# Performance work log

Measured on AMD Instinct MI355X. Metric: run time of the kernel, lower is better.

## Reference

```python
import jax, jax.numpy as jnp
import numpy as np

N = 50000
E = 800000
DIMS = [(8, 16), (16, 16), (16, 16)]  # (in, out) per layer


def setup_inputs() -> dict:
    key = jax.random.key(0)
    ks = jax.random.split(key, 32)
    inp = {}
    inp['x'] = jax.random.normal(ks[0], (N, 8), dtype=jnp.float32)
    inp['pos'] = jax.random.normal(ks[1], (N, 3), dtype=jnp.float32)
    k = 2
    for i, (ci, co) in enumerate(DIMS):
        d = ci * co
        inp[f'lin_w{i}'] = jax.random.normal(ks[k], (3, d), dtype=jnp.float32); k += 1
        inp[f'lin_b{i}'] = jax.random.normal(ks[k], (d,), dtype=jnp.float32); k += 1
        inp[f'gamma{i}'] = jax.random.normal(ks[k], (d,), dtype=jnp.float32); k += 1
        inp[f'beta{i}'] = jax.random.normal(ks[k], (d,), dtype=jnp.float32); k += 1
        inp[f'root{i}'] = jax.random.normal(ks[k], (ci, co), dtype=jnp.float32); k += 1
        inp[f'bias{i}'] = jax.random.normal(ks[k], (co,), dtype=jnp.float32); k += 1
    inp['batch'] = jnp.zeros((N,), dtype=jnp.int32)
    inp['idx'] = jnp.sort(jax.random.randint(ks[k], (25000,), 0, N, dtype=jnp.int32)); k += 1
    inp['edge_index'] = jax.random.randint(ks[k], (2, E), 0, N, dtype=jnp.int32)
    return inp


def _nnconv(x, pseudo, src, dst, lin_w, lin_b, gamma, beta, root, bias, ci, co):
    # edge MLP (Linear -> batchnorm(eval, affine) -> ReLU), plain_last=False
    w = jax.nn.relu((pseudo @ lin_w + lin_b) * gamma + beta)  # [E, ci*co]
    w = w.reshape(-1, ci, co)                                  # [E, ci, co]
    msg = jnp.einsum('ei,eio->eo', x[src], w)                  # per-edge vec-mat
    s = jax.ops.segment_sum(msg, dst, num_segments=N)          # scatter-sum
    cnt = jax.ops.segment_sum(jnp.ones((msg.shape[0],), x.dtype), dst, num_segments=N)
    aggr = s / jnp.maximum(cnt, 1.0)[:, None]                  # scatter-mean
    return aggr + x @ root + bias


def reference(x, pos, lin_w0, lin_b0, gamma0, beta0, root0, bias0,
              lin_w1, lin_b1, gamma1, beta1, root1, bias1,
              lin_w2, lin_b2, gamma2, beta2, root2, bias2,
              batch, idx, edge_index):
    src, dst = edge_index[0], edge_index[1]
    pseudo = pos[dst] - pos[src]  # patch_size is None
    params = [
        (lin_w0, lin_b0, gamma0, beta0, root0, bias0),
        (lin_w1, lin_b1, gamma1, beta1, root1, bias1),
        (lin_w2, lin_b2, gamma2, beta2, root2, bias2),
    ]
    h = x
    for (ci, co), p in zip(DIMS, params):
        h = jax.nn.relu(_nnconv(h, pseudo, src, dst, *p, ci, co))  # drop_act=False
    return h[idx], pos[idx], batch[idx]
```

## Files before the change

### kernel.cpp

```cpp
#include <hip/hip_runtime.h>

#define N_NODES 50000
#define N_EDGES 800000
#define M_IDX   25000
#define DMAX    64

typedef float v2f __attribute__((ext_vector_type(2)));

__global__ __launch_bounds__(256) void prep_kernel(
    const int*   __restrict__ ei,
    const float* __restrict__ pos,
    int*         __restrict__ cnt,
    float4*      __restrict__ pdata,
    const float* __restrict__ lw0, const float* __restrict__ lb0,
    const float* __restrict__ g0,  const float* __restrict__ b0,
    const float* __restrict__ lw1, const float* __restrict__ lb1,
    const float* __restrict__ g1,  const float* __restrict__ b1,
    const float* __restrict__ lw2, const float* __restrict__ lb2,
    const float* __restrict__ g2,  const float* __restrict__ b2,
    float4*      __restrict__ wtab,
    int E)
{
    if (blockIdx.x < 3) {
        const int l = blockIdx.x, j = threadIdx.x;
        const float *lw, *lb, *gm, *bt; int d;
        if (l == 0)      { lw = lw0; lb = lb0; gm = g0; bt = b0; d = 128; }
        else if (l == 1) { lw = lw1; lb = lb1; gm = g1; bt = b1; d = 256; }
        else             { lw = lw2; lb = lb2; gm = g2; bt = b2; d = 256; }
        if (j < d) {
            const float g = gm[j];
            float4 w4;
            w4.x = lw[j] * g;
            w4.y = lw[d + j] * g;
            w4.z = lw[2 * d + j] * g;
            w4.w = fmaf(lb[j], g, bt[j]);
            wtab[l * 256 + j] = w4;
        }
    }

    const int e0 = blockIdx.x * 512 + threadIdx.x;
    const int e1 = e0 + 256;
    const bool v0 = e0 < E, v1 = e1 < E;
    int t0 = 0, s0 = 0, t1 = 0, s1 = 0;
    if (v0) { t0 = ei[E + e0]; s0 = ei[e0]; }
    if (v1) { t1 = ei[E + e1]; s1 = ei[e1]; }
    int p0 = 0, p1 = 0;
    if (v0) p0 = atomicAdd(&cnt[t0], 1);
    if (v1) p1 = atomicAdd(&cnt[t1], 1);
    if (v0) {
        float4 pd;
        pd.x = pos[t0 * 3 + 0] - pos[s0 * 3 + 0];
        pd.y = pos[t0 * 3 + 1] - pos[s0 * 3 + 1];
        pd.z = pos[t0 * 3 + 2] - pos[s0 * 3 + 2];
        pd.w = __int_as_float(s0);
        if (p0 < DMAX) pdata[(size_t)t0 * DMAX + p0] = pd;
    }
    if (v1) {
        float4 pd;
        pd.x = pos[t1 * 3 + 0] - pos[s1 * 3 + 0];
        pd.y = pos[t1 * 3 + 1] - pos[s1 * 3 + 1];
        pd.z = pos[t1 * 3 + 2] - pos[s1 * 3 + 2];
        pd.w = __int_as_float(s1);
        if (p1 < DMAX) pdata[(size_t)t1 * DMAX + p1] = pd;
    }
}

template<int IQ>
__device__ __forceinline__ void load_x(const float* __restrict__ h, int s, int eg, v2f* xv) {
    if constexpr (IQ == 4) {
        float4 v = ((const float4*)h)[s * 4 + eg];
        xv[0] = (v2f){v.x, v.y};
        xv[1] = (v2f){v.z, v.w};
    } else {
        float2 v = ((const float2*)h)[s * 4 + eg];
        xv[0] = (v2f){v.x, v.y};
    }
}

template<int CI>
__global__ __launch_bounds__(256) void node_wave_kernel(
    const float4* __restrict__ pdata,
    const int*    __restrict__ cnt,
    const float*  __restrict__ h_in,
    const float4* __restrict__ wt_l,
    const float*  __restrict__ root,
    const float*  __restrict__ bias,
    float*        __restrict__ h_out,
    int N)
{
    constexpr int IQ = CI / 4;
    constexpr int NP = IQ / 2;
    const int gtid   = blockIdx.x * blockDim.x + threadIdx.x;
    const int wid    = gtid >> 6;
    const int nwaves = (gridDim.x * blockDim.x) >> 6;
    const int lane   = gtid & 63;
    const int eg     = lane >> 4;
    const int o      = lane & 15;

    v2f W0[NP], W1[NP], W2[NP], Bv[NP], Rv[NP];
#pragma unroll
    for (int u = 0; u < NP; ++u) {
        float4 wa = wt_l[(eg * IQ + 2 * u) * 16 + o];
        float4 wb = wt_l[(eg * IQ + 2 * u + 1) * 16 + o];
        W0[u] = (v2f){wa.x, wb.x};
        W1[u] = (v2f){wa.y, wb.y};
        W2[u] = (v2f){wa.z, wb.z};
        Bv[u] = (v2f){wa.w, wb.w};
        Rv[u] = (v2f){root[(eg * IQ + 2 * u) * 16 + o],
                      root[(eg * IQ + 2 * u + 1) * 16 + o]};
    }
    const float bo = bias[o];
    const v2f zero = 0.f;

    for (int t = wid; t < N; t += nwaves) {
        const int deg = cnt[t];
        const int dl  = min(deg, DMAX);
        const float4* __restrict__ row = pdata + (size_t)t * DMAX;

        float4 pdA = row[0], pdB = row[1];
        v2f vacc = 0.f;
        for (int p = 0; p < dl; p += 2) {
            const bool okB = (p + 1) < dl;
            const int sA = __float_as_int(pdA.w);
            const int sB = okB ? __float_as_int(pdB.w) : sA;
            v2f xA[NP], xB[NP];
            load_x<IQ>(h_in, sA, eg, xA);
            load_x<IQ>(h_in, sB, eg, xB);
            const int pn = min(p + 2, DMAX - 2);
            float4 pdA2 = row[pn], pdB2 = row[pn + 1];
            v2f ax = pdA.x, ay = pdA.y, az = pdA.z;
            v2f bx = pdB.x, by = pdB.y, bz = pdB.z;
            v2f eA = 0.f, eB = 0.f;
#pragma unroll
            for (int u = 0; u < NP; ++u) {
                v2f wA = __builtin_elementwise_fma(az, W2[u],
                         __builtin_elementwise_fma(ay, W1[u],
                         __builtin_elementwise_fma(ax, W0[u], Bv[u])));
                wA = __builtin_elementwise_max(wA, zero);
                eA = __builtin_elementwise_fma(xA[u], wA, eA);
                v2f wB = __builtin_elementwise_fma(bz, W2[u],
                         __builtin_elementwise_fma(by, W1[u],
                         __builtin_elementwise_fma(bx, W0[u], Bv[u])));
                wB = __builtin_elementwise_max(wB, zero);
                eB = __builtin_elementwise_fma(xB[u], wB, eB);
            }
            vacc += eA + (okB ? eB : zero);
            pdA = pdA2; pdB = pdB2;
        }
        float acc = vacc.x + vacc.y;

        v2f xT[NP];
        load_x<IQ>(h_in, t, eg, xT);
        v2f rpv = 0.f;
#pragma unroll
        for (int u = 0; u < NP; ++u)
            rpv = __builtin_elementwise_fma(xT[u], Rv[u], rpv);
        float rp = rpv.x + rpv.y;

        float contrib = fmaf(acc, 1.0f / fmaxf((float)deg, 1.0f), rp);
        contrib += __shfl_xor(contrib, 16);
        contrib += __shfl_xor(contrib, 32);

        if (eg == 0) h_out[t * 16 + o] = fmaxf(contrib + bo, 0.f);
    }
}

__global__ __launch_bounds__(256) void gather_kernel(
    const float* __restrict__ h,
    const float* __restrict__ pos,
    const int*   __restrict__ batch,
    const int*   __restrict__ idx,
    float*       __restrict__ out,
    int M)
{
    int j = blockIdx.x * blockDim.x + threadIdx.x;
    if (j >= M) return;
    int n = idx[j];
    float4*       o4 = (float4*)out + (size_t)j * 4;
    const float4* h4 = (const float4*)(h + (size_t)n * 16);
    o4[0] = h4[0]; o4[1] = h4[1]; o4[2] = h4[2]; o4[3] = h4[3];
    float* po = out + (size_t)M * 16 + (size_t)j * 3;
    po[0] = pos[n * 3 + 0];
    po[1] = pos[n * 3 + 1];
    po[2] = pos[n * 3 + 2];
    ((int*)out)[(size_t)M * 19 + j] = batch[n];
}

extern "C" void kernel_launch(void* const* d_in, const int* in_sizes, int n_in,
                              void* d_out, int out_size, void* d_ws, size_t ws_size,
                              hipStream_t stream) {
    const float* x      = (const float*)d_in[0];
    const float* pos    = (const float*)d_in[1];
    const float* lin_w0 = (const float*)d_in[2];
    const float* lin_b0 = (const float*)d_in[3];
    const float* gamma0 = (const float*)d_in[4];
    const float* beta0  = (const float*)d_in[5];
    const float* root0  = (const float*)d_in[6];
    const float* bias0  = (const float*)d_in[7];
    const float* lin_w1 = (const float*)d_in[8];
    const float* lin_b1 = (const float*)d_in[9];
    const float* gamma1 = (const float*)d_in[10];
    const float* beta1  = (const float*)d_in[11];
    const float* root1  = (const float*)d_in[12];
    const float* bias1  = (const float*)d_in[13];
    const float* lin_w2 = (const float*)d_in[14];
    const float* lin_b2 = (const float*)d_in[15];
    const float* gamma2 = (const float*)d_in[16];
    const float* beta2  = (const float*)d_in[17];
    const float* root2  = (const float*)d_in[18];
    const float* bias2  = (const float*)d_in[19];
    const int*   batch  = (const int*)d_in[20];
    const int*   idx    = (const int*)d_in[21];
    const int*   ei     = (const int*)d_in[22];
    float*       out    = (float*)d_out;

    float4* pdata = (float4*)d_ws;
    float*  hA    = (float*)(pdata + (size_t)N_NODES * DMAX);
    float*  hB    = hA + (size_t)N_NODES * 16;
    int*    cnt   = (int*)(hB + (size_t)N_NODES * 16);
    float4* wtab  = (float4*)(cnt + N_NODES);

    hipMemsetAsync(cnt, 0, N_NODES * sizeof(int), stream);
    prep_kernel<<<(N_EDGES + 511) / 512, 256, 0, stream>>>(
        ei, pos, cnt, pdata,
        lin_w0, lin_b0, gamma0, beta0,
        lin_w1, lin_b1, gamma1, beta1,
        lin_w2, lin_b2, gamma2, beta2, wtab, N_EDGES);

    const int NB = 2048;

    node_wave_kernel<8><<<NB, 256, 0, stream>>>(pdata, cnt, x,
        wtab, root0, bias0, hA, N_NODES);
    node_wave_kernel<16><<<NB, 256, 0, stream>>>(pdata, cnt, hA,
        wtab + 256, root1, bias1, hB, N_NODES);
    node_wave_kernel<16><<<NB, 256, 0, stream>>>(pdata, cnt, hB,
        wtab + 512, root2, bias2, hA, N_NODES);

    gather_kernel<<<(M_IDX + 255) / 256, 256, 0, stream>>>(hA, pos, batch, idx, out, M_IDX);
}
```

Before: 324.3 us.

## Process two destination nodes per wavefront, splitting input channels in halves

Each 64-lane wave now handles two nodes at once: lanes are split into two node groups, and each group splits the input channels into two halves instead of four quarters. This halves the wave iterations and removes one cross-lane shuffle. Each lane does twice the per-edge channel work, and the two nodes in a wave may have different degrees, causing divergence. The software prefetch of the next edge pair is dropped in favour of direct loads inside the loop.

```diff
diff --git a/kernel.cpp b/kernel.cpp
--- a/kernel.cpp
+++ b/kernel.cpp
@@ -65,15 +65,14 @@
     }
 }
 
-template<int IQ>
-__device__ __forceinline__ void load_x(const float* __restrict__ h, int s, int eg, v2f* xv) {
-    if constexpr (IQ == 4) {
-        float4 v = ((const float4*)h)[s * 4 + eg];
-        xv[0] = (v2f){v.x, v.y};
-        xv[1] = (v2f){v.z, v.w};
-    } else {
-        float2 v = ((const float2*)h)[s * 4 + eg];
-        xv[0] = (v2f){v.x, v.y};
+template<int NF4>
+__device__ __forceinline__ void load_half(const float4* __restrict__ h4,
+                                          size_t base, v2f* xv) {
+#pragma unroll
+    for (int k = 0; k < NF4; ++k) {
+        float4 v = h4[base + k];
+        xv[2 * k]     = (v2f){v.x, v.y};
+        xv[2 * k + 1] = (v2f){v.z, v.w};
     }
 }
 
@@ -88,46 +87,52 @@
     float*        __restrict__ h_out,
     int N)
 {
-    constexpr int IQ = CI / 4;
-    constexpr int NP = IQ / 2;
+    constexpr int IQ  = CI / 2;
+    constexpr int NP  = IQ / 2;
+    constexpr int F4  = CI / 4;
+    constexpr int NF4 = IQ / 4;
     const int gtid   = blockIdx.x * blockDim.x + threadIdx.x;
     const int wid    = gtid >> 6;
     const int nwaves = (gridDim.x * blockDim.x) >> 6;
     const int lane   = gtid & 63;
-    const int eg     = lane >> 4;
+    const int g      = lane >> 4;
     const int o      = lane & 15;
+    const int nsel   = g >> 1;
+    const int ih     = g & 1;
 
     v2f W0[NP], W1[NP], W2[NP], Bv[NP], Rv[NP];
 #pragma unroll
     for (int u = 0; u < NP; ++u) {
-        float4 wa = wt_l[(eg * IQ + 2 * u) * 16 + o];
-        float4 wb = wt_l[(eg * IQ + 2 * u + 1) * 16 + o];
+        float4 wa = wt_l[(ih * IQ + 2 * u) * 16 + o];
+        float4 wb = wt_l[(ih * IQ + 2 * u + 1) * 16 + o];
         W0[u] = (v2f){wa.x, wb.x};
         W1[u] = (v2f){wa.y, wb.y};
         W2[u] = (v2f){wa.z, wb.z};
         Bv[u] = (v2f){wa.w, wb.w};
-        Rv[u] = (v2f){root[(eg * IQ + 2 * u) * 16 + o],
-                      root[(eg * IQ + 2 * u + 1) * 16 + o]};
+        Rv[u] = (v2f){root[(ih * IQ + 2 * u) * 16 + o],
+                      root[(ih * IQ + 2 * u + 1) * 16 + o]};
     }
     const float bo = bias[o];
     const v2f zero = 0.f;
-
-    for (int t = wid; t < N; t += nwaves) {
+    const float4* __restrict__ h4 = (const float4*)h_in;
+
+    const int NPAIR = N >> 1;
+    for (int tb = wid; tb < NPAIR; tb += nwaves) {
+        const int t   = 2 * tb + nsel;
         const int deg = cnt[t];
         const int dl  = min(deg, DMAX);
         const float4* __restrict__ row = pdata + (size_t)t * DMAX;
 
-        float4 pdA = row[0], pdB = row[1];
         v2f vacc = 0.f;
         for (int p = 0; p < dl; p += 2) {
+            float4 pdA = row[p];
             const bool okB = (p + 1) < dl;
+            float4 pdB = row[okB ? p + 1 : p];
             const int sA = __float_as_int(pdA.w);
-            const int sB = okB ? __float_as_int(pdB.w) : sA;
+            const int sB = __float_as_int(pdB.w);
             v2f xA[NP], xB[NP];
-            load_x<IQ>(h_in, sA, eg, xA);
-            load_x<IQ>(h_in, sB, eg, xB);
-            const int pn = min(p + 2, DMAX - 2);
-            float4 pdA2 = row[pn], pdB2 = row[pn + 1];
+            load_half<NF4>(h4, (size_t)sA * F4 + ih * NF4, xA);
+            load_half<NF4>(h4, (size_t)sB * F4 + ih * NF4, xB);
             v2f ax = pdA.x, ay = pdA.y, az = pdA.z;
             v2f bx = pdB.x, by = pdB.y, bz = pdB.z;
             v2f eA = 0.f, eB = 0.f;
@@ -145,12 +150,11 @@
                 eB = __builtin_elementwise_fma(xB[u], wB, eB);
             }
             vacc += eA + (okB ? eB : zero);
-            pdA = pdA2; pdB = pdB2;
         }
         float acc = vacc.x + vacc.y;
 
         v2f xT[NP];
-        load_x<IQ>(h_in, t, eg, xT);
+        load_half<NF4>(h4, (size_t)t * F4 + ih * NF4, xT);
         v2f rpv = 0.f;
 #pragma unroll
         for (int u = 0; u < NP; ++u)
@@ -159,9 +163,8 @@
 
         float contrib = fmaf(acc, 1.0f / fmaxf((float)deg, 1.0f), rp);
         contrib += __shfl_xor(contrib, 16);
-        contrib += __shfl_xor(contrib, 32);
-
-        if (eg == 0) h_out[t * 16 + o] = fmaxf(contrib + bo, 0.f);
+
+        if ((g & 1) == 0) h_out[t * 16 + o] = fmaxf(contrib + bo, 0.f);
     }
 }
 
```

Result: slower. 346.0 us (+6.7%).
